# Kernel optimization log

Hardware: AMD Instinct MI355X
Metric: run time of the kernel (lower is better)

## Reference

```python
import jax, jax.numpy as jnp
import numpy as np

B, S, D, F, E, K = 2, 2048, 1024, 4096, 8, 2


def setup_inputs() -> dict:
    key = jax.random.key(0)
    ks = jax.random.split(key, 6)
    s = 0.02  # init scale
    return {
        "x": jax.random.normal(ks[0], (B, S, D), dtype=jnp.float32),
        "Wr": jax.random.normal(ks[1], (D, E), dtype=jnp.float32) * s,
        "br": jnp.zeros((E,), dtype=jnp.float32),
        "W1": jax.random.normal(ks[2], (E, D, F), dtype=jnp.float32) * s,
        "b1": jnp.zeros((E, F), dtype=jnp.float32),
        "W2": jax.random.normal(ks[3], (E, F, D), dtype=jnp.float32) * s,
        "b2": jnp.zeros((E, D), dtype=jnp.float32),
        "top_k": K,
    }


def reference(x, Wr, br, W1, b1, W2, b2, top_k):
    b, s, d = x.shape
    e = Wr.shape[1]
    xt = x.reshape(-1, d)                              # [T, D], T = b*s
    logits = xt @ Wr + br                              # [T, E]
    probs = jax.nn.softmax(logits, axis=-1)            # [T, E] router probabilities
    topw, topi = jax.lax.top_k(probs, top_k)           # [T, K] each
    # combine weight per (token, expert): weight if expert in token's top-k else 0
    cw = jnp.sum(jax.nn.one_hot(topi, e, dtype=x.dtype) * topw[..., None], axis=1)  # [T, E]
    # dense grouped FFN: every expert over every token, then weighted combine
    h = jax.nn.relu(jnp.einsum('td,edf->tef', xt, W1) + b1)   # [T, E, F]
    y = jnp.einsum('tef,efd->ted', h, W2) + b2                # [T, E, D]
    out = jnp.einsum('te,ted->td', cw, y).reshape(b, s, d)    # [B, S, D]
    return out, probs.reshape(b, s, e)
```

## Files before the change

### kernel.cpp

```cpp
#include <hip/hip_runtime.h>
#include <hip/hip_bf16.h>


#define T_TOK 4096
#define D_DIM 1024
#define F_DIM 4096
#define E_NUM 8
#define CAP_ROWS 9216
#define N_TILES (CAP_ROWS/128)

typedef __attribute__((ext_vector_type(8))) short short8v;
typedef __attribute__((ext_vector_type(8))) unsigned short ushort8v;
typedef __attribute__((ext_vector_type(4))) float f32x4;

static __device__ __forceinline__ unsigned short f2bf(float f){
  union { float f; unsigned u; } v; v.f = f;
  unsigned r = (v.u + 0x7fffu + ((v.u >> 16) & 1u)) >> 16;
  return (unsigned short)r;
}
static __device__ __forceinline__ float bf2f(unsigned short s){
  union { unsigned u; float f; } v; v.u = ((unsigned)s) << 16;
  return v.f;
}

static __device__ __forceinline__ void gload16(const void* g, void* l) {
  __builtin_amdgcn_global_load_lds(
      (const __attribute__((address_space(1))) unsigned int*)g,
      (__attribute__((address_space(3))) unsigned int*)l, 16, 0, 0);
}

__global__ __launch_bounds__(256) void k_init(int* counts, int* cursor,
                                              int* rows_token, float* rows_w){
  const int gid = blockIdx.x * 256 + threadIdx.x;
  if (gid < E_NUM) counts[gid] = 0;
  else if (gid < 2*E_NUM) cursor[gid - E_NUM] = 0;
  if (gid < CAP_ROWS) { rows_token[gid] = 0; rows_w[gid] = 0.f; }
}

__global__ __launch_bounds__(256) void k_router(
    const float* __restrict__ x, const float* __restrict__ Wr,
    const float* __restrict__ br, float* __restrict__ probs_out,
    int* __restrict__ topi, float* __restrict__ topw, int* __restrict__ counts)
{
  const int lane = threadIdx.x & 63;
  const int t = blockIdx.x * 4 + (threadIdx.x >> 6);
  float xv[16];
  #pragma unroll
  for (int i = 0; i < 16; ++i) xv[i] = x[(size_t)t*D_DIM + i*64 + lane];
  float pe[E_NUM];
  #pragma unroll
  for (int e = 0; e < E_NUM; ++e) {
    float p = 0.f;
    #pragma unroll
    for (int i = 0; i < 16; ++i) p += xv[i] * Wr[(i*64 + lane)*E_NUM + e];
    #pragma unroll
    for (int off = 32; off >= 1; off >>= 1) p += __shfl_xor(p, off);
    pe[e] = p + br[e];
  }
  float m = pe[0];
  #pragma unroll
  for (int e = 1; e < E_NUM; ++e) m = fmaxf(m, pe[e]);
  float s = 0.f;
  #pragma unroll
  for (int e = 0; e < E_NUM; ++e) { pe[e] = expf(pe[e] - m); s += pe[e]; }
  const float inv = 1.f / s;
  int e1 = 0; float v1 = pe[0];
  #pragma unroll
  for (int e = 1; e < E_NUM; ++e) if (pe[e] > v1) { v1 = pe[e]; e1 = e; }
  int e2 = (e1 == 0) ? 1 : 0; float v2 = pe[e2];
  #pragma unroll
  for (int e = 0; e < E_NUM; ++e) if (e != e1 && pe[e] > v2) { v2 = pe[e]; e2 = e; }
  if (lane == 0) {
    #pragma unroll
    for (int e = 0; e < E_NUM; ++e) probs_out[(size_t)t*E_NUM + e] = pe[e] * inv;
    topi[t*2+0] = e1; topw[t*2+0] = v1 * inv;
    topi[t*2+1] = e2; topw[t*2+1] = v2 * inv;
    atomicAdd(&counts[e1], 1);
    atomicAdd(&counts[e2], 1);
  }
}

__global__ void k_scan(const int* __restrict__ counts, int* __restrict__ pbase,
                       int* __restrict__ tile_e)
{
  if (threadIdx.x == 0 && blockIdx.x == 0) {
    int base = 0;
    for (int e = 0; e < E_NUM; ++e) {
      pbase[e] = base;
      const int nt = (counts[e] + 127) >> 7;
      for (int i = 0; i < nt; ++i) tile_e[(base >> 7) + i] = e;
      base += nt << 7;
    }
    pbase[E_NUM] = base;
    for (int tt = base >> 7; tt < N_TILES; ++tt) tile_e[tt] = -1;
  }
}

__global__ __launch_bounds__(256) void k_assign(
    const int* __restrict__ topi, const float* __restrict__ topw,
    const int* __restrict__ pbase, int* __restrict__ cursor,
    int* __restrict__ rows_token, float* __restrict__ rows_w,
    int* __restrict__ pair_of)
{
  const int t = blockIdx.x * 256 + threadIdx.x;
  if (t < T_TOK) {
    #pragma unroll
    for (int k = 0; k < 2; ++k) {
      const int e = topi[t*2+k];
      const int slot = atomicAdd(&cursor[e], 1);
      const int pid = pbase[e] + slot;
      rows_token[pid] = t;
      rows_w[pid] = topw[t*2+k];
      pair_of[t*2+k] = pid;
    }
  }
}

__global__ __launch_bounds__(256) void k_cvt_x(const float* __restrict__ x,
                                               unsigned short* __restrict__ xbf)
{
  const int i = (blockIdx.x * 256 + threadIdx.x) * 4;
  const float4 v = *(const float4*)&x[i];
  ushort4 o; o.x=f2bf(v.x); o.y=f2bf(v.y); o.z=f2bf(v.z); o.w=f2bf(v.w);
  *(ushort4*)&xbf[i] = o;
}

template<int R, int C>
__global__ __launch_bounds__(256) void k_tcvt(const float* __restrict__ in,
                                              unsigned short* __restrict__ out)
{
  const size_t eo = (size_t)blockIdx.z * R * C;
  const int r0 = blockIdx.y * 64, c0 = blockIdx.x * 64;
  __shared__ unsigned short ls[64][66];
  const int t = threadIdx.x;
  const int rr = t >> 4, cc = (t & 15) * 4;
  #pragma unroll
  for (int p = 0; p < 4; ++p) {
    const float4 v = *(const float4*)&in[eo + (size_t)(r0 + p*16 + rr)*C + c0 + cc];
    ls[p*16+rr][cc+0]=f2bf(v.x); ls[p*16+rr][cc+1]=f2bf(v.y);
    ls[p*16+rr][cc+2]=f2bf(v.z); ls[p*16+rr][cc+3]=f2bf(v.w);
  }
  __syncthreads();
  const int kc = (t & 7) * 8, nn0 = t >> 3;
  #pragma unroll
  for (int p = 0; p < 2; ++p) {
    const int nn = nn0 + p*32;
    ushort8v o;
    #pragma unroll
    for (int j = 0; j < 8; ++j) o[j] = ls[kc + j][nn];
    *(ushort8v*)&out[eo + (size_t)(c0 + nn)*R + r0 + kc] = o;
  }
}

template<bool GATHER, int NDIM, int KDIM, bool EPI1>
__global__ __launch_bounds__(256) void k_gemm(
    const unsigned short* __restrict__ A,
    const unsigned short* __restrict__ Bt,
    const float* __restrict__ bias,
    const int* __restrict__ tile_e,
    const int* __restrict__ rows_token,
    const float* __restrict__ rows_w,
    unsigned short* __restrict__ outp)
{
  const int e = tile_e[blockIdx.y];
  if (e < 0) return;
  const int rt = blockIdx.y * 128;
  const int nt = blockIdx.x * 128;
  __shared__ __align__(16) unsigned short As[128*32];
  __shared__ __align__(16) unsigned short Bs[128*32];
  const int tid = threadIdx.x;
  const int lane = tid & 63;
  const int w = tid >> 6;
  const int seg = w & 1;
  const int lrow = lane >> 2, lchunk = lane & 3;
  const unsigned short* gsrc[4];
  unsigned short* ldsd[4];
  if (w < 2) {
    #pragma unroll
    for (int i = 0; i < 4; ++i) {
      const int rl = seg*64 + i*16 + lrow;
      const int rowidx = GATHER ? rows_token[rt + rl] : (rt + rl);
      gsrc[i] = A + (size_t)rowidx * KDIM + lchunk*8;
      ldsd[i] = As + (seg*64 + i*16)*32;
    }
  } else {
    const unsigned short* Be = Bt + (size_t)e * NDIM * KDIM;
    #pragma unroll
    for (int i = 0; i < 4; ++i) {
      const int rl = seg*64 + i*16 + lrow;
      gsrc[i] = Be + (size_t)(nt + rl) * KDIM + lchunk*8;
      ldsd[i] = Bs + (seg*64 + i*16)*32;
    }
  }
  const int wr = w >> 1, wc = w & 1;
  const int cl = lane & 15, rgb = lane >> 4;
  f32x4 acc[4][4] = {};
  for (int k0 = 0; k0 < KDIM; k0 += 32) {
    #pragma unroll
    for (int i = 0; i < 4; ++i) gload16(gsrc[i] + k0, ldsd[i]);
    __syncthreads();
    short8v a[4], b[4];
    #pragma unroll
    for (int m = 0; m < 4; ++m)
      a[m] = *(const short8v*)&As[(wr*64 + m*16 + cl)*32 + rgb*8];
    #pragma unroll
    for (int n = 0; n < 4; ++n)
      b[n] = *(const short8v*)&Bs[(wc*64 + n*16 + cl)*32 + rgb*8];
    #pragma unroll
    for (int m = 0; m < 4; ++m)
      #pragma unroll
      for (int n = 0; n < 4; ++n)
        acc[m][n] = __builtin_amdgcn_mfma_f32_16x16x32_bf16(a[m], b[n], acc[m][n], 0, 0, 0);
    __syncthreads();
  }
  const size_t ebias = (size_t)e * NDIM;
  #pragma unroll
  for (int n = 0; n < 4; ++n) {
    const int col = nt + wc*64 + n*16 + cl;
    const float bv = bias[ebias + col];
    #pragma unroll
    for (int m = 0; m < 4; ++m) {
      const int row = rt + wr*64 + m*16 + rgb*4;
      #pragma unroll
      for (int r = 0; r < 4; ++r) {
        float v = acc[m][n][r] + bv;
        if (EPI1) {
          v = v > 0.f ? v : 0.f;
        } else {
          v *= rows_w[row + r];
        }
        outp[(size_t)(row + r)*NDIM + col] = f2bf(v);
      }
    }
  }
}

__global__ __launch_bounds__(256) void k_combine(
    const unsigned short* __restrict__ y, const int* __restrict__ pair_of,
    float* __restrict__ out)
{
  const int gid = blockIdx.x * 256 + threadIdx.x;
  const int t = gid >> 7;
  const int c = (gid & 127) * 8;
  const int p0 = pair_of[t*2+0];
  const int p1 = pair_of[t*2+1];
  const ushort8v a = *(const ushort8v*)&y[(size_t)p0*D_DIM + c];
  const ushort8v b = *(const ushort8v*)&y[(size_t)p1*D_DIM + c];
  float o[8];
  #pragma unroll
  for (int j = 0; j < 8; ++j) o[j] = bf2f(a[j]) + bf2f(b[j]);
  float4 o0; o0.x=o[0]; o0.y=o[1]; o0.z=o[2]; o0.w=o[3];
  float4 o1; o1.x=o[4]; o1.y=o[5]; o1.z=o[6]; o1.w=o[7];
  *(float4*)&out[(size_t)t*D_DIM + c]     = o0;
  *(float4*)&out[(size_t)t*D_DIM + c + 4] = o1;
}

extern "C" void kernel_launch(void* const* d_in, const int* in_sizes, int n_in,
                              void* d_out, int out_size, void* d_ws, size_t ws_size,
                              hipStream_t stream)
{
  const float* x  = (const float*)d_in[0];
  const float* Wr = (const float*)d_in[1];
  const float* br = (const float*)d_in[2];
  const float* W1 = (const float*)d_in[3];
  const float* b1 = (const float*)d_in[4];
  const float* W2 = (const float*)d_in[5];
  const float* b2 = (const float*)d_in[6];
  (void)in_sizes; (void)n_in; (void)out_size; (void)ws_size;

  float* out   = (float*)d_out;
  float* probs = out + (size_t)T_TOK * D_DIM;

  char* w = (char*)d_ws;
  size_t off = 0;
  int*   counts     = (int*)(w + off); off += 256;
  int*   cursor     = (int*)(w + off); off += 256;
  int*   pbase      = (int*)(w + off); off += 512;
  int*   tile_e     = (int*)(w + off); off += 3072;
  int*   topi       = (int*)(w + off); off += (size_t)T_TOK*2*4;
  float* topw       = (float*)(w + off); off += (size_t)T_TOK*2*4;
  int*   pair_of    = (int*)(w + off); off += (size_t)T_TOK*2*4;
  int*   rows_token = (int*)(w + off); off += (size_t)CAP_ROWS*4;
  float* rows_w     = (float*)(w + off); off += (size_t)CAP_ROWS*4;
  off = (off + 255) & ~(size_t)255;
  unsigned short* xbf = (unsigned short*)(w + off); off += (size_t)T_TOK*D_DIM*2;
  unsigned short* Wt  = (unsigned short*)(w + off); off += (size_t)E_NUM*D_DIM*F_DIM*2;
  unsigned short* h   = (unsigned short*)(w + off); off += (size_t)CAP_ROWS*F_DIM*2;
  unsigned short* y   = (unsigned short*)(w + off); off += (size_t)CAP_ROWS*D_DIM*2;

  k_init<<<(CAP_ROWS + 255) / 256, 256, 0, stream>>>(counts, cursor, rows_token, rows_w);
  k_router<<<T_TOK / 4, 256, 0, stream>>>(x, Wr, br, probs, topi, topw, counts);
  k_scan<<<1, 64, 0, stream>>>(counts, pbase, tile_e);
  k_assign<<<T_TOK / 256, 256, 0, stream>>>(topi, topw, pbase, cursor,
                                            rows_token, rows_w, pair_of);
  k_cvt_x<<<T_TOK * D_DIM / 4 / 256, 256, 0, stream>>>(x, xbf);
  k_tcvt<D_DIM, F_DIM><<<dim3(F_DIM/64, D_DIM/64, E_NUM), 256, 0, stream>>>(W1, Wt);
  k_gemm<true, F_DIM, D_DIM, true><<<dim3(F_DIM/128, N_TILES), 256, 0, stream>>>(
      xbf, Wt, b1, tile_e, rows_token, rows_w, h);
  k_tcvt<F_DIM, D_DIM><<<dim3(D_DIM/64, F_DIM/64, E_NUM), 256, 0, stream>>>(W2, Wt);
  k_gemm<false, D_DIM, F_DIM, false><<<dim3(D_DIM/128, N_TILES), 256, 0, stream>>>(
      h, Wt, b2, tile_e, rows_token, rows_w, y);
  k_combine<<<T_TOK * D_DIM / 8 / 256, 256, 0, stream>>>(y, pair_of, out);
}
```

Measured before the change: 513.2 us.

## Triple-buffer LDS tiles with async global loads in MoE grouped GEMM

```diff
diff --git a/kernel.cpp b/kernel.cpp
--- a/kernel.cpp
+++ b/kernel.cpp
@@ -153,7 +153,7 @@
 }
 
 template<bool GATHER, int NDIM, int KDIM, bool EPI1>
-__global__ __launch_bounds__(256) void k_gemm(
+__global__ __launch_bounds__(256, 2) void k_gemm(
     const unsigned short* __restrict__ A,
     const unsigned short* __restrict__ Bt,
     const float* __restrict__ bias,
@@ -165,58 +165,78 @@
   const int e = tile_e[blockIdx.y];
   if (e < 0) return;
   const int rt = blockIdx.y * 128;
-  const int nt = blockIdx.x * 128;
-  __shared__ __align__(16) unsigned short As[128*32];
-  __shared__ __align__(16) unsigned short Bs[128*32];
+  const int ntc = blockIdx.x * 128;
+  __shared__ __align__(16) unsigned short LB[3][2][128*32];
   const int tid = threadIdx.x;
   const int lane = tid & 63;
   const int w = tid >> 6;
   const int seg = w & 1;
+  const int isB = (w >= 2) ? 1 : 0;
   const int lrow = lane >> 2, lchunk = lane & 3;
   const unsigned short* gsrc[4];
-  unsigned short* ldsd[4];
+  unsigned lds_off[4];
   if (w < 2) {
     #pragma unroll
     for (int i = 0; i < 4; ++i) {
       const int rl = seg*64 + i*16 + lrow;
       const int rowidx = GATHER ? rows_token[rt + rl] : (rt + rl);
       gsrc[i] = A + (size_t)rowidx * KDIM + lchunk*8;
-      ldsd[i] = As + (seg*64 + i*16)*32;
+      lds_off[i] = (unsigned)((seg*64 + i*16)*32);
     }
   } else {
     const unsigned short* Be = Bt + (size_t)e * NDIM * KDIM;
     #pragma unroll
     for (int i = 0; i < 4; ++i) {
       const int rl = seg*64 + i*16 + lrow;
-      gsrc[i] = Be + (size_t)(nt + rl) * KDIM + lchunk*8;
-      ldsd[i] = Bs + (seg*64 + i*16)*32;
+      gsrc[i] = Be + (size_t)(ntc + rl) * KDIM + lchunk*8;
+      lds_off[i] = (unsigned)((seg*64 + i*16)*32);
     }
   }
   const int wr = w >> 1, wc = w & 1;
   const int cl = lane & 15, rgb = lane >> 4;
   f32x4 acc[4][4] = {};
-  for (int k0 = 0; k0 < KDIM; k0 += 32) {
-    #pragma unroll
-    for (int i = 0; i < 4; ++i) gload16(gsrc[i] + k0, ldsd[i]);
-    __syncthreads();
+
+  constexpr int NT = KDIM / 32;
+  #pragma unroll
+  for (int i = 0; i < 4; ++i) gload16(gsrc[i] + 0,  &LB[0][isB][lds_off[i]]);
+  #pragma unroll
+  for (int i = 0; i < 4; ++i) gload16(gsrc[i] + 32, &LB[1][isB][lds_off[i]]);
+  asm volatile("s_waitcnt vmcnt(4)" ::: "memory");
+  __builtin_amdgcn_s_barrier();
+
+  int buf = 0;
+  for (int t = 0; t < NT; ++t) {
+    const int pb = (buf == 0) ? 2 : (buf - 1);
+    if (t + 2 < NT) {
+      const int kof = (t + 2) * 32;
+      #pragma unroll
+      for (int i = 0; i < 4; ++i) gload16(gsrc[i] + kof, &LB[pb][isB][lds_off[i]]);
+    }
     short8v a[4], b[4];
     #pragma unroll
     for (int m = 0; m < 4; ++m)
-      a[m] = *(const short8v*)&As[(wr*64 + m*16 + cl)*32 + rgb*8];
+      a[m] = *(const short8v*)&LB[buf][0][(wr*64 + m*16 + cl)*32 + rgb*8];
     #pragma unroll
     for (int n = 0; n < 4; ++n)
-      b[n] = *(const short8v*)&Bs[(wc*64 + n*16 + cl)*32 + rgb*8];
+      b[n] = *(const short8v*)&LB[buf][1][(wc*64 + n*16 + cl)*32 + rgb*8];
     #pragma unroll
     for (int m = 0; m < 4; ++m)
       #pragma unroll
       for (int n = 0; n < 4; ++n)
         acc[m][n] = __builtin_amdgcn_mfma_f32_16x16x32_bf16(a[m], b[n], acc[m][n], 0, 0, 0);
-    __syncthreads();
-  }
+    if (t + 2 < NT) {
+      asm volatile("s_waitcnt vmcnt(4)" ::: "memory");
+    } else {
+      asm volatile("s_waitcnt vmcnt(0)" ::: "memory");
+    }
+    __builtin_amdgcn_s_barrier();
+    buf = (buf == 2) ? 0 : (buf + 1);
+  }
+
   const size_t ebias = (size_t)e * NDIM;
   #pragma unroll
   for (int n = 0; n < 4; ++n) {
-    const int col = nt + wc*64 + n*16 + cl;
+    const int col = ntc + wc*64 + n*16 + cl;
     const float bv = bias[ebias + col];
     #pragma unroll
     for (int m = 0; m < 4; ++m) {
@@ -224,12 +244,14 @@
       #pragma unroll
       for (int r = 0; r < 4; ++r) {
         float v = acc[m][n][r] + bv;
-        if (EPI1) {
-          v = v > 0.f ? v : 0.f;
-        } else {
-          v *= rows_w[row + r];
+        if (EPI1) v = fmaxf(v, 0.f);
+        else      v *= rows_w[row + r];
+        const unsigned short hb = f2bf(v);
+        const unsigned short ob = (unsigned short)__shfl_xor((int)(unsigned)hb, 1);
+        if ((lane & 1) == 0) {
+          const unsigned pk = (unsigned)hb | ((unsigned)ob << 16);
+          *(unsigned*)&outp[(size_t)(row + r)*NDIM + col] = pk;
         }
-        outp[(size_t)(row + r)*NDIM + col] = f2bf(v);
       }
     }
   }
```

Result: faster. 466.5 us (-9.1%).
